# Kernel tuning notes

Hardware: AMD Instinct MI355X
Metric: run time of the kernel (lower is better)

## Reference

```python
import jax, jax.numpy as jnp
import numpy as np

B, H, W, D = 8, 64, 64, 512
NH, DK = 16, 32
WS, SH = 8, 4            # window size, shift size = WS // 2
L = 4                    # n_layer
WS2 = WS * WS
NWH, NWW = H // WS, W // WS
SCALE = 1.0 / np.sqrt(DK)


def _rel_index(ws):
    # standard Swin relative position index: (ws^2, ws^2) into a (2ws-1)^2 table
    coords = np.stack(np.meshgrid(np.arange(ws), np.arange(ws), indexing='ij'))
    cf = coords.reshape(2, -1)
    rel = cf[:, :, None] - cf[:, None, :] + (ws - 1)
    return (rel[0] * (2 * ws - 1) + rel[1]).astype(np.int32)


def _shift_mask():
    # Swin-style shifted-window attention mask for cyclic shift by SH
    img = np.zeros((H, W), dtype=np.int32)
    cnt = 0
    sls = (slice(0, -WS), slice(-WS, -SH), slice(-SH, None))
    for hs in sls:
        for ws_ in sls:
            img[hs, ws_] = cnt
            cnt += 1
    win = img.reshape(NWH, WS, NWW, WS).transpose(0, 2, 1, 3).reshape(NWH, NWW, WS2)
    m = win[..., None, :] != win[..., :, None]          # (nh, nw, ws2, ws2)
    return np.broadcast_to(m[None, None], (1, NH, NWH, NWW, WS2, WS2)).copy()


def setup_inputs() -> dict:
    key = jax.random.key(0)
    ks = jax.random.split(key, 12)
    s = 0.02
    inp = {
        'x': jax.random.normal(ks[0], (B, H, W, D), jnp.float32),
        'mask': jnp.asarray(_shift_mask()),
        'rel_index': jnp.asarray(_rel_index(WS)),
        'Wq': jax.random.normal(ks[1], (L, D, D), jnp.float32) * s,
        'bq': jnp.zeros((L, D), jnp.float32),
        'Wkv': jax.random.normal(ks[2], (L, D, 2 * D), jnp.float32) * s,
        'bkv': jnp.zeros((L, 2 * D), jnp.float32),
        'Wo': jax.random.normal(ks[3], (L, D, D), jnp.float32) * s,
        'bo': jnp.zeros((L, D), jnp.float32),
        'rel_table': jax.random.normal(ks[4], (L, (2 * WS - 1) ** 2, NH), jnp.float32) * s,
        'ln1_g': jnp.ones((L, D), jnp.float32),
        'ln1_b': jnp.zeros((L, D), jnp.float32),
        'ln2_g': jnp.ones((L, D), jnp.float32),
        'ln2_b': jnp.zeros((L, D), jnp.float32),
        'W1': jax.random.normal(ks[5], (L, D, 4 * D), jnp.float32) * s,
        'b1': jnp.zeros((L, 4 * D), jnp.float32),
        'W2': jax.random.normal(ks[6], (L, 4 * D, D), jnp.float32) * s,
        'b2': jnp.zeros((L, D), jnp.float32),
    }
    return inp


def _ln(x, g, b):
    m = jnp.mean(x, -1, keepdims=True)
    v = jnp.mean(jnp.square(x - m), -1, keepdims=True)
    return (x - m) * jax.lax.rsqrt(v + 1e-5) * g + b


def _partition(t):
    # (B,H,W,NH,DK) -> (B,NH,nh,nw,ws^2,DK)
    t = t.reshape(B, NWH, WS, NWW, WS, NH, DK)
    return t.transpose(0, 5, 1, 3, 2, 4, 6).reshape(B, NH, NWH, NWW, WS2, DK)


def _merge(t):
    # (B,NH,nh,nw,ws^2,DK) -> (B,H,W,NH,DK)
    t = t.reshape(B, NH, NWH, NWW, WS, WS, DK).transpose(0, 2, 4, 3, 5, 1, 6)
    return t.reshape(B, H, W, NH, DK)


def _attn(xn, mask, rel_index, Wq, bq, Wkv, bkv, Wo, bo, table):
    q = (xn @ Wq + bq).reshape(B, H, W, NH, DK)
    kv = (xn @ Wkv + bkv).reshape(B, H, W, 2, NH, DK)
    k, v = kv[..., 0, :, :], kv[..., 1, :, :]
    # cyclic shift (shifting=True since n_class=4)
    q = jnp.roll(q, (-SH, -SH), axis=(1, 2))
    k = jnp.roll(k, (-SH, -SH), axis=(1, 2))
    v = jnp.roll(v, (-SH, -SH), axis=(1, 2))
    qw, kw, vw = _partition(q), _partition(k), _partition(v)
    scores = jnp.einsum('bhnmqd,bhnmkd->bhnmqk', qw, kw) * SCALE
    bias = table[rel_index]                      # (ws2, ws2, NH)
    scores = scores + bias.transpose(2, 0, 1)[None, :, None, None]
    scores = jnp.where(mask, -1e9, scores)
    a = jax.nn.softmax(scores, axis=-1)
    o = jnp.einsum('bhnmqk,bhnmkd->bhnmqd', a, vw)
    o = _merge(o)
    o = jnp.roll(o, (SH, SH), axis=(1, 2))       # reverse cyclic shift
    return o.reshape(B, H, W, D) @ Wo + bo


def reference(x, mask, rel_index, Wq, bq, Wkv, bkv, Wo, bo, rel_table,
              ln1_g, ln1_b, ln2_g, ln2_b, W1, b1, W2, b2):
    for i in range(L):
        x = x + _attn(_ln(x, ln1_g[i], ln1_b[i]), mask, rel_index,
                      Wq[i], bq[i], Wkv[i], bkv[i], Wo[i], bo[i], rel_table[i])
        h = _ln(x, ln2_g[i], ln2_b[i])
        x = x + (jax.nn.gelu(h @ W1[i] + b1[i]) @ W2[i] + b2[i])
    return x
```

## Files before the change

kernel.cpp:

```cpp
#include <hip/hip_runtime.h>
#include <hip/hip_bf16.h>

typedef __hip_bfloat16 bf16;
typedef __attribute__((ext_vector_type(8))) short short8;
typedef __attribute__((ext_vector_type(4))) float f32x4;

#define GLDS16(g, l) __builtin_amdgcn_global_load_lds(                              \
    (__attribute__((address_space(1))) const void*)(g),                             \
    (__attribute__((address_space(3))) void*)(l), 16, 0, 0)

#define SCALE_ 0.17677669529663687f

__global__ void detect_k(const unsigned int* __restrict__ ln1g_raw, int* __restrict__ flag)
{
    if (threadIdx.x == 0) *flag = (ln1g_raw[0] == 0x3F803F80u) ? 0 : 1;
}

__global__ __launch_bounds__(256)
void cvt_small_k(const void* __restrict__ src, bf16* __restrict__ dst, const int n,
                 const int* __restrict__ flag)
{
    const int i = blockIdx.x * 256 + threadIdx.x;
    if (i >= n) return;
    const bool f32 = (*flag != 0);
    dst[i] = f32 ? (bf16)((const float*)src)[i] : ((const bf16*)src)[i];
}

__global__ void transpose2_k(const float* __restrict__ inF, const bf16* __restrict__ inB,
                             bf16* __restrict__ out, const int R, const int C,
                             const int* __restrict__ flag)
{
    __shared__ bf16 tile[32][33];
    const bool f32 = (*flag != 0);
    const int c0 = blockIdx.x * 32, r0 = blockIdx.y * 32;
    const int tx = threadIdx.x, ty = threadIdx.y;
#pragma unroll
    for (int k = 0; k < 4; k++) {
        const long idx = (long)(r0 + ty + k * 8) * C + c0 + tx;
        tile[ty + k * 8][tx] = f32 ? (bf16)inF[idx] : inB[idx];
    }
    __syncthreads();
#pragma unroll
    for (int k = 0; k < 4; k++)
        out[(long)(c0 + ty + k * 8) * R + r0 + tx] = tile[tx][ty + k * 8];
}

__device__ __forceinline__ float gelu_f(float v)
{
    const float u = 0.7978845608028654f * (v + 0.044715f * v * v * v);
    const float e = __expf(-2.0f * u);
    return v * __builtin_amdgcn_rcpf(1.0f + e);
}

#define SBAR()   __builtin_amdgcn_s_barrier()
#define SCHED0() __builtin_amdgcn_sched_barrier(0)
#define WLGKM()  { asm volatile("s_waitcnt lgkmcnt(0)"); SCHED0(); }

template <int EPI>
__global__ __launch_bounds__(512, 2)
void gemm256(const bf16* __restrict__ A, const bf16* __restrict__ Bt,
             const bf16* __restrict__ bias0, const bf16* __restrict__ bias1,
             const int split,
             bf16* __restrict__ outb, float* __restrict__ outf,
             const int M, const int N, const int K)
{
    __shared__ char smem[131072] __attribute__((aligned(16)));

    const int nT  = N >> 8;
    const int nwg = gridDim.x;
    const int bid = blockIdx.x;
    const int wg = (bid & 7) * (nwg >> 3) + (bid >> 3);
    const int mb = wg / nT;
    const int nb = wg - mb * nT;
    const int m0 = mb << 8, n0 = nb << 8;

    const int tid  = threadIdx.x;
    const int lane = tid & 63;
    const int wave = tid >> 6;
    const int wm = wave >> 2;
    const int wn = wave & 3;
    const int fr  = lane & 15;
    const int oct = lane >> 4;
    const int l8  = lane >> 3;
    const int cx  = (lane & 7) ^ l8;

    const int T = K >> 6;

    const bf16* Asrc = A  + (long)(m0 + wm * 128 + wn * 32 + l8) * K + cx * 8;
    char*       Adst = smem + wm * 16384 + wn * 4096;
    const int h    = wn >> 1;
    const int bsub = wm * 2 + (wn & 1);
    const bf16* Bsrc = Bt + (long)(n0 + h * 128 + bsub * 32 + l8) * K + cx * 8;
    char*       Bdst = smem + 65536 + h * 16384 + bsub * 4096;

#define STAGE_A(kt, p) {                                                   \
        const bf16* s_ = Asrc + (long)(kt) * 64;                           \
        char* d_ = Adst + (p) * 32768;                                     \
        GLDS16(s_,            d_);                                         \
        GLDS16(s_ +  8L * K,  d_ + 1024);                                  \
        GLDS16(s_ + 16L * K,  d_ + 2048);                                  \
        GLDS16(s_ + 24L * K,  d_ + 3072); }
#define STAGE_B(kt, p) {                                                   \
        const bf16* s_ = Bsrc + (long)(kt) * 64;                           \
        char* d_ = Bdst + (p) * 32768;                                     \
        GLDS16(s_,            d_);                                         \
        GLDS16(s_ +  8L * K,  d_ + 1024);                                  \
        GLDS16(s_ + 16L * K,  d_ + 2048);                                  \
        GLDS16(s_ + 24L * K,  d_ + 3072); }

    const int kx0 = (     oct * 16) ^ ((fr & 7) << 4);
    const int kx1 = (64 + oct * 16) ^ ((fr & 7) << 4);
    const int aoff = (wm * 128 + fr) * 128;
    const int boff = 65536 + (wn * 64 + fr) * 128;

    f32x4 acc[8][4];
#pragma unroll
    for (int m = 0; m < 8; m++)
#pragma unroll
        for (int n = 0; n < 4; n++) acc[m][n] = (f32x4){0.f, 0.f, 0.f, 0.f};

    short8 af[4][2], bf[4][2];

    STAGE_B(0, 0); STAGE_A(0, 0);
    STAGE_B(1, 1); STAGE_A(1, 1);
    SCHED0();
    asm volatile("s_waitcnt vmcnt(8)");
    SCHED0();
    SBAR();

    for (int t = 0; t < T; ++t) {
        const int pOff = (t & 1) << 15;

#pragma unroll
        for (int mm = 0; mm < 4; mm++) {
            af[mm][0] = *(const short8*)(smem + pOff + aoff + mm * 2048 + kx0);
            af[mm][1] = *(const short8*)(smem + pOff + aoff + mm * 2048 + kx1);
        }
#pragma unroll
        for (int nn = 0; nn < 2; nn++) {
            bf[nn][0] = *(const short8*)(smem + pOff + boff + nn * 2048 + kx0);
            bf[nn][1] = *(const short8*)(smem + pOff + boff + nn * 2048 + kx1);
        }
        SBAR();
        WLGKM();
        __builtin_amdgcn_s_setprio(1);
#pragma unroll
        for (int ks = 0; ks < 2; ks++)
#pragma unroll
            for (int mm = 0; mm < 4; mm++)
#pragma unroll
                for (int nn = 0; nn < 2; nn++)
                    acc[mm][nn] = __builtin_amdgcn_mfma_f32_16x16x32_bf16(
                        bf[nn][ks], af[mm][ks], acc[mm][nn], 0, 0, 0);
        __builtin_amdgcn_s_setprio(0);
        SBAR();

#pragma unroll
        for (int nn = 2; nn < 4; nn++) {
            bf[nn][0] = *(const short8*)(smem + pOff + boff + nn * 2048 + kx0);
            bf[nn][1] = *(const short8*)(smem + pOff + boff + nn * 2048 + kx1);
        }
        SBAR();
        WLGKM();
        __builtin_amdgcn_s_setprio(1);
#pragma unroll
        for (int ks = 0; ks < 2; ks++)
#pragma unroll
            for (int mm = 0; mm < 4; mm++)
#pragma unroll
                for (int nn = 2; nn < 4; nn++)
                    acc[mm][nn] = __builtin_amdgcn_mfma_f32_16x16x32_bf16(
                        bf[nn][ks], af[mm][ks], acc[mm][nn], 0, 0, 0);
        __builtin_amdgcn_s_setprio(0);
        SBAR();

#pragma unroll
        for (int mm = 0; mm < 4; mm++) {
            af[mm][0] = *(const short8*)(smem + pOff + aoff + (4 + mm) * 2048 + kx0);
            af[mm][1] = *(const short8*)(smem + pOff + aoff + (4 + mm) * 2048 + kx1);
        }
        if (t < T - 2) STAGE_B(t + 2, (t & 1));
        SBAR();
        WLGKM();
        __builtin_amdgcn_s_setprio(1);
#pragma unroll
        for (int ks = 0; ks < 2; ks++)
#pragma unroll
            for (int mm = 0; mm < 4; mm++)
#pragma unroll
                for (int nn = 2; nn < 4; nn++)
                    acc[4 + mm][nn] = __builtin_amdgcn_mfma_f32_16x16x32_bf16(
                        bf[nn][ks], af[mm][ks], acc[4 + mm][nn], 0, 0, 0);
        __builtin_amdgcn_s_setprio(0);
        SBAR();

        if (t < T - 2) STAGE_A(t + 2, (t & 1));
        __builtin_amdgcn_s_setprio(1);
#pragma unroll
        for (int ks = 0; ks < 2; ks++)
#pragma unroll
            for (int mm = 0; mm < 4; mm++)
#pragma unroll
                for (int nn = 0; nn < 2; nn++)
                    acc[4 + mm][nn] = __builtin_amdgcn_mfma_f32_16x16x32_bf16(
                        bf[nn][ks], af[mm][ks], acc[4 + mm][nn], 0, 0, 0);
        __builtin_amdgcn_s_setprio(0);
        SCHED0();
        if (t < T - 2)       { asm volatile("s_waitcnt vmcnt(8)"); }
        else if (t == T - 2) { asm volatile("s_waitcnt vmcnt(0)"); }
        SCHED0();
        SBAR();
    }
#undef STAGE_A
#undef STAGE_B

    if (EPI == 2) {
        const int erow = m0 + wm * 128 + fr;
        const int ecol = n0 + wn * 64 + (oct << 2);
#pragma unroll
        for (int nn = 0; nn < 4; nn++) {
            const int col0 = ecol + nn * 16;
            const bf16* bp = (col0 < split) ? (bias0 + col0) : (bias1 + (col0 - split));
            const float bv0 = (float)bp[0], bv1 = (float)bp[1];
            const float bv2 = (float)bp[2], bv3 = (float)bp[3];
#pragma unroll
            for (int mm = 0; mm < 8; mm++) {
                const long base = (long)(erow + mm * 16) * N + col0;
                float4 o = *(const float4*)(outf + base);
                o.x += acc[mm][nn][0] + bv0;
                o.y += acc[mm][nn][1] + bv1;
                o.z += acc[mm][nn][2] + bv2;
                o.w += acc[mm][nn][3] + bv3;
                *(float4*)(outf + base) = o;
            }
        }
    } else {
        const int col_l = wn * 64 + (oct << 2);
#pragma unroll
        for (int nn = 0; nn < 4; nn++) {
            const int cl = col_l + nn * 16;
            const int cg = n0 + cl;
            const bf16* bp = (cg < split) ? (bias0 + cg) : (bias1 + (cg - split));
            const float bv0 = (float)bp[0], bv1 = (float)bp[1];
            const float bv2 = (float)bp[2], bv3 = (float)bp[3];
#pragma unroll
            for (int mm = 0; mm < 8; mm++) {
                const int row_l = wm * 128 + mm * 16 + fr;
                float v0 = acc[mm][nn][0] + bv0;
                float v1 = acc[mm][nn][1] + bv1;
                float v2 = acc[mm][nn][2] + bv2;
                float v3 = acc[mm][nn][3] + bv3;
                if (EPI == 1) { v0 = gelu_f(v0); v1 = gelu_f(v1); v2 = gelu_f(v2); v3 = gelu_f(v3); }
                union { ushort4 u; bf16 hh[4]; } pk;
                pk.hh[0] = (bf16)v0; pk.hh[1] = (bf16)v1;
                pk.hh[2] = (bf16)v2; pk.hh[3] = (bf16)v3;
                int ad = (row_l << 9) + (cl << 1);
                ad ^= ((row_l & 7) << 4);
                *(ushort4*)(smem + ad) = pk.u;
            }
        }
        asm volatile("s_waitcnt lgkmcnt(0)");
        SBAR();
        const int rgrp = tid >> 5;
        const int chnk = tid & 31;
#pragma unroll
        for (int rr = 0; rr < 16; rr++) {
            const int row_l = rgrp * 16 + rr;
            int ad = (row_l << 9) + (chnk << 4);
            ad ^= ((row_l & 7) << 4);
            const uint4 val = *(const uint4*)(smem + ad);
            *(uint4*)((char*)outb + ((long)(m0 + row_l) * N + n0) * 2 + (chnk << 4)) = val;
        }
    }
}

__global__ __launch_bounds__(256)
void ln_k(const float* __restrict__ x, const bf16* __restrict__ g,
          const bf16* __restrict__ b, bf16* __restrict__ out)
{
    const int token = blockIdx.x * 4 + (threadIdx.x >> 6);
    const int lane  = threadIdx.x & 63;
    const float* xp = x + (long)token * 512 + lane * 8;
    float4 u0 = ((const float4*)xp)[0];
    float4 u1 = ((const float4*)xp)[1];
    float v[8] = {u0.x, u0.y, u0.z, u0.w, u1.x, u1.y, u1.z, u1.w};
    float s = 0.f, ss = 0.f;
#pragma unroll
    for (int e = 0; e < 8; e++) { s += v[e]; ss += v[e] * v[e]; }
#pragma unroll
    for (int off = 1; off < 64; off <<= 1) {
        s  += __shfl_xor(s,  off);
        ss += __shfl_xor(ss, off);
    }
    const float mean = s * (1.0f / 512.0f);
    const float var  = ss * (1.0f / 512.0f) - mean * mean;
    const float rstd = rsqrtf(var + 1e-5f);
    union { uint4 u; bf16 h[8]; } gg, bb, oo;
    gg.u = *(const uint4*)(g + lane * 8);
    bb.u = *(const uint4*)(b + lane * 8);
#pragma unroll
    for (int e = 0; e < 8; e++)
        oo.h[e] = (bf16)((v[e] - mean) * rstd * (float)gg.h[e] + (float)bb.h[e]);
    *(uint4*)(out + (long)token * 512 + lane * 8) = oo.u;
}

__global__ __launch_bounds__(64)
void bias_pre_k(const bf16* __restrict__ table, float* __restrict__ biasF)
{
    const int blk = blockIdx.x;
    const int q = blk & 63, n = (blk >> 6) & 15, c = blk >> 10;
    const int j = threadIdx.x;
    const int ri = q >> 3, ci = q & 7, rj = j >> 3, cj = j & 7;
    const float bias = (float)table[((ri - rj + 7) * 15 + (ci - cj + 7)) * 16 + n];
    const int shi = (c & 1) ? (ri < 4 ? 1 : 2) : 0;
    const int shj = (c & 1) ? (rj < 4 ? 1 : 2) : 0;
    const int swi = (c & 2) ? (ci < 4 ? 1 : 2) : 0;
    const int swj = (c & 2) ? (cj < 4 ? 1 : 2) : 0;
    biasF[((long)blk << 6) + j] = ((shi != shj) || (swi != swj)) ? -1.0e9f : bias;
}

__global__ __launch_bounds__(64, 3)
void attn_k2(const bf16* __restrict__ qkv, const float* __restrict__ biasF,
             bf16* __restrict__ out)
{
    __shared__ char lds[12800];
    const int bid = blockIdx.x;
    const int n  = bid & 15;
    const int ww = (bid >> 4) & 7;
    const int wh = (bid >> 7) & 7;
    const int b  = bid >> 10;
    const int lane = threadIdx.x;
    const int fr  = lane & 15;
    const int oct = lane >> 4;
    const int cls = ((wh == 7) ? 1 : 0) | ((ww == 7) ? 2 : 0);

    {
        const int d  = lane & 31;
        const int jh = lane >> 5;
        const long Ce = (((long)b * 64 + wh * 8 + 4) * 64 + (ww * 8 + 4)) * 1536;
        const long hsub = (wh == 7) ? 6291456L : 0L;
        const long wsub = (ww == 7) ? 98304L   : 0L;
        const long vbase = Ce + 1024 + n * 32 + d;
        long rowb[4];
#pragma unroll
        for (int qq = 0; qq < 4; qq++) {
            const int r = jh * 4 + qq;
            rowb[qq] = vbase + (long)r * 98304 - (r >= 4 ? hsub : 0);
        }
        union { ushort us[8]; uint4 u4; } vg[4];
#pragma unroll
        for (int c = 0; c < 32; c++) {
            const int qq = c >> 3, cj = c & 7;
            const long a = rowb[qq] + (long)cj * 1536 - (cj >= 4 ? wsub : 0);
            vg[qq].us[cj] = *(const ushort*)(qkv + a);
        }
#pragma unroll
        for (int qq = 0; qq < 4; qq++)
            *(uint4*)(lds + d * 144 + jh * 64 + qq * 16) = vg[qq].u4;
    }

    long tok[4];
#pragma unroll
    for (int tt = 0; tt < 4; tt++) {
        const int j = fr + 16 * tt;
        const int rj = j >> 3, cj = j & 7;
        const int gh = (wh * 8 + rj + 4) & 63;
        const int gw = (ww * 8 + cj + 4) & 63;
        tok[tt] = ((long)b * 64 + gh) * 64 + gw;
    }

    short8 kf[4];
#pragma unroll
    for (int t = 0; t < 4; t++)
        kf[t] = *(const short8*)(qkv + tok[t] * 1536 + 512 + n * 32 + oct * 8);

    const float* biasW = biasF + (((long)(cls * 16 + n)) << 12);
    float inv[4];
#pragma unroll
    for (int mm = 0; mm < 4; mm++) {
        const short8 qf = *(const short8*)(qkv + tok[mm] * 1536 + n * 32 + oct * 8);
        f32x4 sv[4];
#pragma unroll
        for (int nn = 0; nn < 4; nn++)
            sv[nn] = __builtin_amdgcn_mfma_f32_16x16x32_bf16(
                kf[nn], qf, (f32x4){0.f, 0.f, 0.f, 0.f}, 0, 0, 0);
        float p[16];
        float mx = -3.0e38f;
#pragma unroll
        for (int nn = 0; nn < 4; nn++) {
            const f32x4 bz = *(const f32x4*)(biasW + ((fr + 16 * mm) << 6) + nn * 16 + oct * 4);
#pragma unroll
            for (int r = 0; r < 4; r++) {
                p[nn * 4 + r] = sv[nn][r] * SCALE_ + bz[r];
                mx = fmaxf(mx, p[nn * 4 + r]);
            }
        }
        mx = fmaxf(mx, __shfl_xor(mx, 16));
        mx = fmaxf(mx, __shfl_xor(mx, 32));
        float sum = 0.f;
#pragma unroll
        for (int e = 0; e < 16; e++) { p[e] = __expf(p[e] - mx); sum += p[e]; }
        sum += __shfl_xor(sum, 16);
        sum += __shfl_xor(sum, 32);
        inv[mm] = __builtin_amdgcn_rcpf(sum);

        const int prow = 4608 + ((fr + 16 * mm) << 7);
#pragma unroll
        for (int nn = 0; nn < 4; nn++) {
            union { bf16 h[2]; unsigned u; } lo, hi;
            lo.h[0] = (bf16)p[nn * 4 + 0]; lo.h[1] = (bf16)p[nn * 4 + 1];
            hi.h[0] = (bf16)p[nn * 4 + 2]; hi.h[1] = (bf16)p[nn * 4 + 3];
            uint2 w; w.x = lo.u; w.y = hi.u;
            *(uint2*)(lds + prow + ((nn * 32 + oct * 8) ^ ((fr & 7) << 4))) = w;
        }
    }

    f32x4 oa[4][2];
#pragma unroll
    for (int mm = 0; mm < 4; mm++)
#pragma unroll
        for (int nd = 0; nd < 2; nd++) oa[mm][nd] = (f32x4){0.f, 0.f, 0.f, 0.f};
#pragma unroll
    for (int kc = 0; kc < 2; kc++) {
        const short8 vt0 = *(const short8*)(lds + fr * 144        + kc * 64 + oct * 16);
        const short8 vt1 = *(const short8*)(lds + (fr + 16) * 144 + kc * 64 + oct * 16);
#pragma unroll
        for (int mm = 0; mm < 4; mm++) {
            const short8 pf = *(const short8*)(lds + 4608 + ((fr + 16 * mm) << 7)
                                  + ((kc * 64 + oct * 16) ^ ((fr & 7) << 4)));
            oa[mm][0] = __builtin_amdgcn_mfma_f32_16x16x32_bf16(vt0, pf, oa[mm][0], 0, 0, 0);
            oa[mm][1] = __builtin_amdgcn_mfma_f32_16x16x32_bf16(vt1, pf, oa[mm][1], 0, 0, 0);
        }
    }

#pragma unroll
    for (int mm = 0; mm < 4; mm++) {
        bf16* op = out + tok[mm] * 512 + n * 32 + oct * 4;
#pragma unroll
        for (int nd = 0; nd < 2; nd++) {
            union { ushort4 u; bf16 h[4]; } o4;
#pragma unroll
            for (int r = 0; r < 4; r++) o4.h[r] = (bf16)(oa[mm][nd][r] * inv[mm]);
            *(ushort4*)(op + nd * 16) = o4.u;
        }
    }
}

__global__ __launch_bounds__(256)
void x2f_k(const void* __restrict__ in, float* __restrict__ out, const long n8,
           const int* __restrict__ flag)
{
    const long idx = (long)blockIdx.x * 256 + threadIdx.x;
    if (idx >= n8) return;
    if (*flag != 0) {
        ((float4*)out)[idx * 2]     = ((const float4*)in)[idx * 2];
        ((float4*)out)[idx * 2 + 1] = ((const float4*)in)[idx * 2 + 1];
    } else {
        union { uint4 u; bf16 h[8]; } t;
        t.u = ((const uint4*)in)[idx];
        ((float4*)out)[idx * 2] =
            make_float4((float)t.h[0], (float)t.h[1], (float)t.h[2], (float)t.h[3]);
        ((float4*)out)[idx * 2 + 1] =
            make_float4((float)t.h[4], (float)t.h[5], (float)t.h[6], (float)t.h[7]);
    }
}

__global__ __launch_bounds__(256)
void copyout_k(const float* __restrict__ in, float* __restrict__ out, const long n8)
{
    const long idx = (long)blockIdx.x * 256 + threadIdx.x;
    if (idx >= n8) return;
    ((float4*)out)[idx * 2]     = ((const float4*)in)[idx * 2];
    ((float4*)out)[idx * 2 + 1] = ((const float4*)in)[idx * 2 + 1];
}

extern "C" void kernel_launch(void* const* d_in, const int* in_sizes, int n_in,
                              void* d_out, int out_size, void* d_ws, size_t ws_size,
                              hipStream_t stream)
{
    const void* x_in = d_in[0];
    const void* Wq   = d_in[3];
    const void* bq   = d_in[4];
    const void* Wkv  = d_in[5];
    const void* bkv  = d_in[6];
    const void* Wo   = d_in[7];
    const void* bo   = d_in[8];
    const void* rtab = d_in[9];
    const void* ln1g = d_in[10];
    const void* ln1b = d_in[11];
    const void* ln2g = d_in[12];
    const void* ln2b = d_in[13];
    const void* W1   = d_in[14];
    const void* b1   = d_in[15];
    const void* W2   = d_in[16];
    const void* b2   = d_in[17];

    if (ws_size < (size_t)260046848) return;

    char* ws = (char*)d_ws;
    float* bufX   = (float*)(ws);
    bf16*  bufXN  = (bf16*)(ws + 67108864);
    bf16*  bufQKV = (bf16*)(ws + 100663296);
    bf16*  bufMLP = bufQKV;
    bf16*  bufATT = (bf16*)(ws + 201326592);
    bf16*  wT     = (bf16*)(ws + 234881024);

    int*  flag = (int*)d_out;
    bf16* pp   = (bf16*)((char*)d_out + 256);
    bf16* p_bq   = pp;
    bf16* p_bkv  = pp + 2048;
    bf16* p_bo   = pp + 6144;
    bf16* p_rtab = pp + 8192;
    bf16* p_l1g  = pp + 22592;
    bf16* p_l1b  = pp + 24640;
    bf16* p_l2g  = pp + 26688;
    bf16* p_l2b  = pp + 28736;
    bf16* p_b1   = pp + 30784;
    bf16* p_b2   = pp + 38976;
    float* biasAll = (float*)((char*)d_out + 33554432);

    const long LSTR = 3145728;

    detect_k<<<1, 64, 0, stream>>>((const unsigned int*)ln1g, flag);

    cvt_small_k<<<8,  256, 0, stream>>>(bq,   p_bq,   2048,  flag);
    cvt_small_k<<<16, 256, 0, stream>>>(bkv,  p_bkv,  4096,  flag);
    cvt_small_k<<<8,  256, 0, stream>>>(bo,   p_bo,   2048,  flag);
    cvt_small_k<<<57, 256, 0, stream>>>(rtab, p_rtab, 14400, flag);
    cvt_small_k<<<8,  256, 0, stream>>>(ln1g, p_l1g,  2048,  flag);
    cvt_small_k<<<8,  256, 0, stream>>>(ln1b, p_l1b,  2048,  flag);
    cvt_small_k<<<8,  256, 0, stream>>>(ln2g, p_l2g,  2048,  flag);
    cvt_small_k<<<8,  256, 0, stream>>>(ln2b, p_l2b,  2048,  flag);
    cvt_small_k<<<32, 256, 0, stream>>>(b1,   p_b1,   8192,  flag);
    cvt_small_k<<<8,  256, 0, stream>>>(b2,   p_b2,   2048,  flag);

    for (int i = 0; i < 4; i++)
        bias_pre_k<<<4096, 64, 0, stream>>>(p_rtab + i * 3600, biasAll + (long)i * 262144);

    for (int i = 0; i < 4; i++) {
        bf16* wl = wT + (long)i * LSTR;
        transpose2_k<<<dim3(16,16), dim3(32,8), 0, stream>>>(
            (const float*)Wq  + (long)i*262144,  (const bf16*)Wq  + (long)i*262144,
            wl,           512,  512, flag);
        transpose2_k<<<dim3(32,16), dim3(32,8), 0, stream>>>(
            (const float*)Wkv + (long)i*524288,  (const bf16*)Wkv + (long)i*524288,
            wl + 262144,  512, 1024, flag);
        transpose2_k<<<dim3(16,16), dim3(32,8), 0, stream>>>(
            (const float*)Wo  + (long)i*262144,  (const bf16*)Wo  + (long)i*262144,
            wl + 786432,  512,  512, flag);
        transpose2_k<<<dim3(64,16), dim3(32,8), 0, stream>>>(
            (const float*)W1  + (long)i*1048576, (const bf16*)W1  + (long)i*1048576,
            wl + 1048576, 512, 2048, flag);
        transpose2_k<<<dim3(16,64), dim3(32,8), 0, stream>>>(
            (const float*)W2  + (long)i*1048576, (const bf16*)W2  + (long)i*1048576,
            wl + 2097152, 2048, 512, flag);
    }
    x2f_k<<<8192, 256, 0, stream>>>(x_in, bufX, (long)2097152, flag);

    for (int i = 0; i < 4; i++) {
        const bf16* wl = wT + (long)i * LSTR;
        ln_k<<<8192, 256, 0, stream>>>(bufX, p_l1g + i*512, p_l1b + i*512, bufXN);
        gemm256<0><<<768, 512, 0, stream>>>(bufXN, wl, p_bq + i*512, p_bkv + i*1024, 512,
                                            bufQKV, nullptr, 32768, 1536, 512);
        attn_k2<<<8192, 64, 0, stream>>>(bufQKV, biasAll + (long)i * 262144, bufATT);
        gemm256<2><<<256, 512, 0, stream>>>(bufATT, wl + 786432, p_bo + i*512, p_bo + i*512, 512,
                                            nullptr, bufX, 32768, 512, 512);
        ln_k<<<8192, 256, 0, stream>>>(bufX, p_l2g + i*512, p_l2b + i*512, bufXN);
        gemm256<1><<<1024, 512, 0, stream>>>(bufXN, wl + 1048576, p_b1 + i*2048, p_b1 + i*2048, 2048,
                                             bufMLP, nullptr, 32768, 2048, 512);
        gemm256<2><<<256, 512, 0, stream>>>(bufMLP, wl + 2097152, p_b2 + i*512, p_b2 + i*512, 512,
                                            nullptr, bufX, 32768, 512, 2048);
    }
    copyout_k<<<8192, 256, 0, stream>>>(bufX, (float*)d_out, (long)2097152);
}
```

Before: 1.745 ms.

## Fuse input conversion into first LN and final residual GEMM into output write

Removes the separate x-to-float conversion kernel by having the first layer norm also write the fp32 residual copy, and removes the final copy-out kernel by having the last down-projection GEMM write directly to the output buffer. Because d_out is overwritten while it holds the staged bf16 params, b2 is reconverted into workspace scratch before the last GEMM. Also adds scheduling barriers around LDS loads and staging in the GEMM main loop. This saves two full-tensor memory passes at the cost of a small extra conversion launch and some added code complexity.

```diff
diff --git a/kernel.cpp b/kernel.cpp
--- a/kernel.cpp
+++ b/kernel.cpp
@@ -62,6 +62,7 @@
              const bf16* __restrict__ bias0, const bf16* __restrict__ bias1,
              const int split,
              bf16* __restrict__ outb, float* __restrict__ outf,
+             float* __restrict__ outf2,
              const int M, const int N, const int K)
 {
     __shared__ char smem[131072] __attribute__((aligned(16)));
@@ -141,6 +142,7 @@
             bf[nn][0] = *(const short8*)(smem + pOff + boff + nn * 2048 + kx0);
             bf[nn][1] = *(const short8*)(smem + pOff + boff + nn * 2048 + kx1);
         }
+        SCHED0();
         SBAR();
         WLGKM();
         __builtin_amdgcn_s_setprio(1);
@@ -153,6 +155,7 @@
                     acc[mm][nn] = __builtin_amdgcn_mfma_f32_16x16x32_bf16(
                         bf[nn][ks], af[mm][ks], acc[mm][nn], 0, 0, 0);
         __builtin_amdgcn_s_setprio(0);
+        SCHED0();
         SBAR();
 
 #pragma unroll
@@ -160,6 +163,7 @@
             bf[nn][0] = *(const short8*)(smem + pOff + boff + nn * 2048 + kx0);
             bf[nn][1] = *(const short8*)(smem + pOff + boff + nn * 2048 + kx1);
         }
+        SCHED0();
         SBAR();
         WLGKM();
         __builtin_amdgcn_s_setprio(1);
@@ -172,6 +176,7 @@
                     acc[mm][nn] = __builtin_amdgcn_mfma_f32_16x16x32_bf16(
                         bf[nn][ks], af[mm][ks], acc[mm][nn], 0, 0, 0);
         __builtin_amdgcn_s_setprio(0);
+        SCHED0();
         SBAR();
 
 #pragma unroll
@@ -179,7 +184,9 @@
             af[mm][0] = *(const short8*)(smem + pOff + aoff + (4 + mm) * 2048 + kx0);
             af[mm][1] = *(const short8*)(smem + pOff + aoff + (4 + mm) * 2048 + kx1);
         }
+        SCHED0();
         if (t < T - 2) STAGE_B(t + 2, (t & 1));
+        SCHED0();
         SBAR();
         WLGKM();
         __builtin_amdgcn_s_setprio(1);
@@ -192,9 +199,11 @@
                     acc[4 + mm][nn] = __builtin_amdgcn_mfma_f32_16x16x32_bf16(
                         bf[nn][ks], af[mm][ks], acc[4 + mm][nn], 0, 0, 0);
         __builtin_amdgcn_s_setprio(0);
+        SCHED0();
         SBAR();
 
         if (t < T - 2) STAGE_A(t + 2, (t & 1));
+        SCHED0();
         __builtin_amdgcn_s_setprio(1);
 #pragma unroll
         for (int ks = 0; ks < 2; ks++)
@@ -214,7 +223,7 @@
 #undef STAGE_A
 #undef STAGE_B
 
-    if (EPI == 2) {
+    if (EPI >= 2) {
         const int erow = m0 + wm * 128 + fr;
         const int ecol = n0 + wn * 64 + (oct << 2);
 #pragma unroll
@@ -231,7 +240,8 @@
                 o.y += acc[mm][nn][1] + bv1;
                 o.z += acc[mm][nn][2] + bv2;
                 o.w += acc[mm][nn][3] + bv3;
-                *(float4*)(outf + base) = o;
+                if (EPI == 2) *(float4*)(outf  + base) = o;
+                else          *(float4*)(outf2 + base) = o;
             }
         }
     } else {
@@ -304,6 +314,49 @@
     *(uint4*)(out + (long)token * 512 + lane * 8) = oo.u;
 }
 
+__global__ __launch_bounds__(256)
+void lnx_k(const void* __restrict__ xin, const bf16* __restrict__ g,
+           const bf16* __restrict__ b, float* __restrict__ xf,
+           bf16* __restrict__ out, const int* __restrict__ flag)
+{
+    const int token = blockIdx.x * 4 + (threadIdx.x >> 6);
+    const int lane  = threadIdx.x & 63;
+    float v[8];
+    if (*flag != 0) {
+        const float* xp = (const float*)xin + (long)token * 512 + lane * 8;
+        float4 u0 = ((const float4*)xp)[0];
+        float4 u1 = ((const float4*)xp)[1];
+        v[0] = u0.x; v[1] = u0.y; v[2] = u0.z; v[3] = u0.w;
+        v[4] = u1.x; v[5] = u1.y; v[6] = u1.z; v[7] = u1.w;
+    } else {
+        union { uint4 u; bf16 h[8]; } t;
+        t.u = *(const uint4*)((const bf16*)xin + (long)token * 512 + lane * 8);
+#pragma unroll
+        for (int e = 0; e < 8; e++) v[e] = (float)t.h[e];
+    }
+    float* xo = xf + (long)token * 512 + lane * 8;
+    ((float4*)xo)[0] = make_float4(v[0], v[1], v[2], v[3]);
+    ((float4*)xo)[1] = make_float4(v[4], v[5], v[6], v[7]);
+    float s = 0.f, ss = 0.f;
+#pragma unroll
+    for (int e = 0; e < 8; e++) { s += v[e]; ss += v[e] * v[e]; }
+#pragma unroll
+    for (int off = 1; off < 64; off <<= 1) {
+        s  += __shfl_xor(s,  off);
+        ss += __shfl_xor(ss, off);
+    }
+    const float mean = s * (1.0f / 512.0f);
+    const float var  = ss * (1.0f / 512.0f) - mean * mean;
+    const float rstd = rsqrtf(var + 1e-5f);
+    union { uint4 u; bf16 h[8]; } gg, bb, oo;
+    gg.u = *(const uint4*)(g + lane * 8);
+    bb.u = *(const uint4*)(b + lane * 8);
+#pragma unroll
+    for (int e = 0; e < 8; e++)
+        oo.h[e] = (bf16)((v[e] - mean) * rstd * (float)gg.h[e] + (float)bb.h[e]);
+    *(uint4*)(out + (long)token * 512 + lane * 8) = oo.u;
+}
+
 __global__ __launch_bounds__(64)
 void bias_pre_k(const bf16* __restrict__ table, float* __restrict__ biasF)
 {
@@ -444,34 +497,6 @@
             *(ushort4*)(op + nd * 16) = o4.u;
         }
     }
-}
-
-__global__ __launch_bounds__(256)
-void x2f_k(const void* __restrict__ in, float* __restrict__ out, const long n8,
-           const int* __restrict__ flag)
-{
-    const long idx = (long)blockIdx.x * 256 + threadIdx.x;
-    if (idx >= n8) return;
-    if (*flag != 0) {
-        ((float4*)out)[idx * 2]     = ((const float4*)in)[idx * 2];
-        ((float4*)out)[idx * 2 + 1] = ((const float4*)in)[idx * 2 + 1];
-    } else {
-        union { uint4 u; bf16 h[8]; } t;
-        t.u = ((const uint4*)in)[idx];
-        ((float4*)out)[idx * 2] =
-            make_float4((float)t.h[0], (float)t.h[1], (float)t.h[2], (float)t.h[3]);
-        ((float4*)out)[idx * 2 + 1] =
-            make_float4((float)t.h[4], (float)t.h[5], (float)t.h[6], (float)t.h[7]);
-    }
-}
-
-__global__ __launch_bounds__(256)
-void copyout_k(const float* __restrict__ in, float* __restrict__ out, const long n8)
-{
-    const long idx = (long)blockIdx.x * 256 + threadIdx.x;
-    if (idx >= n8) return;
-    ((float4*)out)[idx * 2]     = ((const float4*)in)[idx * 2];
-    ((float4*)out)[idx * 2 + 1] = ((const float4*)in)[idx * 2 + 1];
 }
 
 extern "C" void kernel_launch(void* const* d_in, const int* in_sizes, int n_in,
@@ -504,6 +529,7 @@
     bf16*  bufMLP = bufQKV;
     bf16*  bufATT = (bf16*)(ws + 201326592);
     bf16*  wT     = (bf16*)(ws + 234881024);
+    bf16*  p_b2w  = (bf16*)(ws + 100663296 - 4096);
 
     int*  flag = (int*)d_out;
     bf16* pp   = (bf16*)((char*)d_out + 256);
@@ -555,21 +581,28 @@
             (const float*)W2  + (long)i*1048576, (const bf16*)W2  + (long)i*1048576,
             wl + 2097152, 2048, 512, flag);
     }
-    x2f_k<<<8192, 256, 0, stream>>>(x_in, bufX, (long)2097152, flag);
 
     for (int i = 0; i < 4; i++) {
         const bf16* wl = wT + (long)i * LSTR;
-        ln_k<<<8192, 256, 0, stream>>>(bufX, p_l1g + i*512, p_l1b + i*512, bufXN);
+        if (i == 0)
+            lnx_k<<<8192, 256, 0, stream>>>(x_in, p_l1g, p_l1b, bufX, bufXN, flag);
+        else
+            ln_k<<<8192, 256, 0, stream>>>(bufX, p_l1g + i*512, p_l1b + i*512, bufXN);
         gemm256<0><<<768, 512, 0, stream>>>(bufXN, wl, p_bq + i*512, p_bkv + i*1024, 512,
-                                            bufQKV, nullptr, 32768, 1536, 512);
+                                            bufQKV, nullptr, nullptr, 32768, 1536, 512);
         attn_k2<<<8192, 64, 0, stream>>>(bufQKV, biasAll + (long)i * 262144, bufATT);
         gemm256<2><<<256, 512, 0, stream>>>(bufATT, wl + 786432, p_bo + i*512, p_bo + i*512, 512,
-                                            nullptr, bufX, 32768, 512, 512);
+                                            nullptr, bufX, nullptr, 32768, 512, 512);
         ln_k<<<8192, 256, 0, stream>>>(bufX, p_l2g + i*512, p_l2b + i*512, bufXN);
         gemm256<1><<<1024, 512, 0, stream>>>(bufXN, wl + 1048576, p_b1 + i*2048, p_b1 + i*2048, 2048,
-                                             bufMLP, nullptr, 32768, 2048, 512);
-        gemm256<2><<<256, 512, 0, stream>>>(bufMLP, wl + 2097152, p_b2 + i*512, p_b2 + i*512, 512,
-                                            nullptr, bufX, 32768, 512, 2048);
-    }
-    copyout_k<<<8192, 256, 0, stream>>>(bufX, (float*)d_out, (long)2097152);
-}
+                                             bufMLP, nullptr, nullptr, 32768, 2048, 512);
+        if (i < 3) {
+            gemm256<2><<<256, 512, 0, stream>>>(bufMLP, wl + 2097152, p_b2 + i*512, p_b2 + i*512, 512,
+                                                nullptr, bufX, nullptr, 32768, 512, 2048);
+        } else {
+            cvt_small_k<<<8, 256, 0, stream>>>(b2, p_b2w, 2048, flag);
+            gemm256<3><<<256, 512, 0, stream>>>(bufMLP, wl + 2097152, p_b2w + 1536, p_b2w + 1536, 512,
+                                                nullptr, bufX, (float*)d_out, 32768, 512, 2048);
+        }
+    }
+}
```

New measurement: 1.743 ms. No clear change (-0.1%).
